# Kernel tuning notes

Hardware: AMD Instinct MI355X
Metric: run time of the kernel (lower is better)

Reference implementation:

```python
import jax, jax.numpy as jnp
import numpy as np

N, C, P, K = 100000, 64, 64, 16  # points, in_planes, planes, nsample
EPS = 1e-5

def _bn(y, g, b, m, v):
    # inference-mode batchnorm over channel (last) dim
    return (y - m) * (g * jax.lax.rsqrt(v + EPS)) + b

def setup_inputs() -> dict:
    key = jax.random.key(0)
    ks = jax.random.split(key, 12)
    p = jax.random.normal(ks[0], (N, 3), jnp.float32)
    x = jax.random.normal(ks[1], (N, C), jnp.float32)
    idx = jax.random.randint(ks[2], (N, K), 0, N, jnp.int32)
    s = 0.05
    w1 = jax.random.normal(ks[3], (C, P), jnp.float32) * s
    conv_w = jax.random.normal(ks[4], (P, P + 3), jnp.float32) * s  # Conv1d(P+3, P, 1) weight squeezed
    w3 = jax.random.normal(ks[5], (P, P), jnp.float32) * s
    def bn_params(k):
        k1, k2 = jax.random.split(k)
        return (jnp.ones((P,), jnp.float32),                      # gamma
                jnp.zeros((P,), jnp.float32),                     # beta
                jax.random.normal(k1, (P,), jnp.float32) * 0.01,  # running mean
                jnp.abs(jax.random.normal(k2, (P,), jnp.float32)) * 0.1 + 1.0)  # running var
    g1, b1, m1, v1 = bn_params(ks[6])
    g2, b2, m2, v2 = bn_params(ks[7])
    g3, b3, m3, v3 = bn_params(ks[8])
    return dict(p=p, x=x, idx=idx, w1=w1, g1=g1, b1=b1, m1=m1, v1=v1,
                conv_w=conv_w, g2=g2, b2=b2, m2=m2, v2=v2,
                w3=w3, g3=g3, b3=b3, m3=m3, v3=v3)

def reference(p, x, idx, w1, g1, b1, m1, v1, conv_w, g2, b2, m2, v2, w3, g3, b3, m3, v3):
    identity = x
    h = jax.nn.relu(_bn(x @ w1, g1, b1, m1, v1))                     # [N, P]
    # queryandgroup with use_xyz=True: concat(relative xyz, neighbor feats)
    rel = p[idx] - p[:, None, :]                                      # [N, K, 3]
    grouped = jnp.concatenate([rel, h[idx]], axis=-1)                 # [N, K, 3+P]
    e = jnp.einsum('nkc,oc->nko', grouped, conv_w)                    # conv1x1 -> [N, K, P]
    e = jax.nn.relu(_bn(e, g2, b2, m2, v2))
    f = jnp.max(e, axis=1)                                            # max over neighbors -> [N, P]
    out = jax.nn.relu(_bn(f @ w3, g3, b3, m3, v3) + identity)         # [N, P]
    return out
```

## Files before the change

kernel.cpp:

```cpp
#include <hip/hip_runtime.h>
#include <stdint.h>


#define EPS 1e-5f

typedef unsigned short u16;
typedef unsigned int u32;
typedef __attribute__((ext_vector_type(8))) short bf16x8;
typedef __attribute__((ext_vector_type(4))) float f32x4;

__device__ __forceinline__ float b2f(u16 u) { return __uint_as_float(((u32)u) << 16); }
__device__ __forceinline__ u16 f2b(float f) {
    u32 u = __float_as_uint(f);
    u32 r = u + 0x7fffu + ((u >> 16) & 1u);
    return (u16)(r >> 16);
}
__device__ __forceinline__ bool is_bf16(const void* g) { return ((const u32*)g)[0] == 0x3F803F80u; }
__device__ __forceinline__ float ldval(const void* p, size_t i, bool isbf) {
    return isbf ? b2f(((const u16*)p)[i]) : ((const float*)p)[i];
}
#define MFMA16(a, b, c) __builtin_amdgcn_mfma_f32_16x16x32_bf16(a, b, c, 0, 0, 0)

__device__ __forceinline__ bf16x8 asbf(uint4 u) {
    union { uint4 u; bf16x8 b; } c;
    c.u = u;
    return c.b;
}

__device__ __forceinline__ bf16x8 ldrow8(const void* base, size_t row, int coff, bool isbf) {
    if (isbf) {
        const u16* pp = (const u16*)base + row * 64 + coff;
        return asbf(*(const uint4*)pp);
    } else {
        const float* pp = (const float*)base + row * 64 + coff;
        float4 q0 = ((const float4*)pp)[0], q1 = ((const float4*)pp)[1];
        bf16x8 r;
        r[0] = (short)f2b(q0.x); r[1] = (short)f2b(q0.y);
        r[2] = (short)f2b(q0.z); r[3] = (short)f2b(q0.w);
        r[4] = (short)f2b(q1.x); r[5] = (short)f2b(q1.y);
        r[6] = (short)f2b(q1.z); r[7] = (short)f2b(q1.w);
        return r;
    }
}

__global__ void __launch_bounds__(256)
k_prep(const void* __restrict__ w1, const void* __restrict__ cw, const void* __restrict__ w3,
       const void* __restrict__ g1, const void* __restrict__ b1, const void* __restrict__ m1,
       const void* __restrict__ v1, const void* __restrict__ g2, const void* __restrict__ b2,
       const void* __restrict__ m2, const void* __restrict__ v2, const void* __restrict__ g3,
       const void* __restrict__ b3, const void* __restrict__ m3, const void* __restrict__ v3,
       uint4* __restrict__ w1f, uint4* __restrict__ cwf, uint4* __restrict__ w3f,
       float* __restrict__ bnst) {
    const bool isbf = is_bf16(g1);
    const int tid = blockIdx.x * blockDim.x + threadIdx.x;
    if (tid < 512) {
        int f = tid >> 6, lane = tid & 63;
        int ch = f >> 2, t = f & 3, quad = lane >> 4, c0 = lane & 15;
        union { uint4 u; bf16x8 b; } r;
#pragma unroll
        for (int j = 0; j < 8; ++j) {
            int c = ch * 32 + quad * 8 + j, o = t * 16 + c0;
            r.b[j] = (short)f2b(ldval(w1, (size_t)c * 64 + o, isbf));
        }
        w1f[f * 64 + lane] = r.u;
    } else if (tid < 1280) {
        int f = (tid - 512) >> 6, lane = tid & 63;
        int ch = f >> 2, t = f & 3, quad = lane >> 4, c0 = lane & 15;
        union { uint4 u; bf16x8 b; } r;
#pragma unroll
        for (int j = 0; j < 8; ++j) {
            int o = t * 16 + c0;
            short val;
            if (ch < 2) {
                int c = ch * 32 + quad * 8 + j;
                val = (short)f2b(ldval(cw, (size_t)o * 67 + 3 + c, isbf));
            } else {
                int pc = quad * 8 + j;
                val = (pc < 3) ? (short)f2b(ldval(cw, (size_t)o * 67 + pc, isbf)) : (short)0;
            }
            r.b[j] = val;
        }
        cwf[f * 64 + lane] = r.u;
    } else if (tid < 1792) {
        int f = (tid - 1280) >> 6, lane = tid & 63;
        int ch = f >> 2, t = f & 3, quad = lane >> 4, c0 = lane & 15;
        union { uint4 u; bf16x8 b; } r;
#pragma unroll
        for (int j = 0; j < 8; ++j) {
            int c = ch * 32 + quad * 8 + j, o = t * 16 + c0;
            r.b[j] = (short)f2b(ldval(w3, (size_t)c * 64 + o, isbf));
        }
        w3f[f * 64 + lane] = r.u;
    } else if (tid < 2176) {
        int id = tid - 1792;
        int bn = id >> 7, rem = id & 127, ch = rem & 63, which = rem >> 6;
        const void* g = (bn == 0) ? g1 : (bn == 1) ? g2 : g3;
        const void* b = (bn == 0) ? b1 : (bn == 1) ? b2 : b3;
        const void* m = (bn == 0) ? m1 : (bn == 1) ? m2 : m3;
        const void* v = (bn == 0) ? v1 : (bn == 1) ? v2 : v3;
        float gv = ldval(g, ch, isbf), bv = ldval(b, ch, isbf);
        float mv = ldval(m, ch, isbf), vv = ldval(v, ch, isbf);
        float s = gv * rsqrtf(vv + EPS);
        float t = bv - mv * s;
        bnst[bn * 128 + which * 64 + ch] = which ? t : s;
    }
}

__global__ void __launch_bounds__(256, 4)
k_h_mfma(const void* __restrict__ x, const void* __restrict__ p, const void* __restrict__ g1,
         const uint4* __restrict__ w1f, const float* __restrict__ bnst,
         float4* __restrict__ p4, u16* __restrict__ hbf, int N) {
    const bool isbf = is_bf16(g1);
    const int lane = threadIdx.x & 63, quad = lane >> 4, col = lane & 15;
    const int wave = blockIdx.x * (blockDim.x >> 6) + (threadIdx.x >> 6);
    const int nw = gridDim.x * (blockDim.x >> 6);
    bf16x8 B00 = asbf(w1f[0 * 64 + lane]), B01 = asbf(w1f[1 * 64 + lane]);
    bf16x8 B02 = asbf(w1f[2 * 64 + lane]), B03 = asbf(w1f[3 * 64 + lane]);
    bf16x8 B10 = asbf(w1f[4 * 64 + lane]), B11 = asbf(w1f[5 * 64 + lane]);
    bf16x8 B12 = asbf(w1f[6 * 64 + lane]), B13 = asbf(w1f[7 * 64 + lane]);
    f32x4 sv, tv;
#pragma unroll
    for (int t = 0; t < 4; ++t) {
        sv[t] = bnst[0 * 128 + 0 + t * 16 + col];
        tv[t] = bnst[0 * 128 + 64 + t * 16 + col];
    }
    const int nt = (N + 15) >> 4;
    for (int ti = wave; ti < nt; ti += nw) {
        const int n0 = ti * 16;
        int ra = n0 + col;
        if (ra > N - 1) ra = N - 1;
        bf16x8 A0 = ldrow8(x, (size_t)ra, quad * 8, isbf);
        bf16x8 A1 = ldrow8(x, (size_t)ra, 32 + quad * 8, isbf);
        if (p4 && quad == 0 && n0 + col < N) {
            int row = n0 + col;
            float4 pv;
            pv.x = ldval(p, (size_t)row * 3 + 0, isbf);
            pv.y = ldval(p, (size_t)row * 3 + 1, isbf);
            pv.z = ldval(p, (size_t)row * 3 + 2, isbf);
            pv.w = 0.f;
            p4[row] = pv;
        }
        f32x4 acc0 = {0.f, 0.f, 0.f, 0.f}, acc1 = acc0, acc2 = acc0, acc3 = acc0;
        acc0 = MFMA16(A0, B00, acc0); acc0 = MFMA16(A1, B10, acc0);
        acc1 = MFMA16(A0, B01, acc1); acc1 = MFMA16(A1, B11, acc1);
        acc2 = MFMA16(A0, B02, acc2); acc2 = MFMA16(A1, B12, acc2);
        acc3 = MFMA16(A0, B03, acc3); acc3 = MFMA16(A1, B13, acc3);
#define STT(acc, t)                                                            \
    {                                                                          \
        _Pragma("unroll") for (int r = 0; r < 4; ++r) {                        \
            int row = n0 + quad * 4 + r;                                       \
            if (row < N) {                                                     \
                float e = acc[r] * sv[t] + tv[t];                              \
                hbf[(size_t)row * 64 + (t)*16 + col] = f2b(fmaxf(e, 0.f));     \
            }                                                                  \
        }                                                                      \
    }
        STT(acc0, 0) STT(acc1, 1) STT(acc2, 2) STT(acc3, 3)
#undef STT
    }
}

__global__ void __launch_bounds__(256, 4)
k_w_mfma(u16* __restrict__ hw, u16* __restrict__ vbuf, const void* __restrict__ p,
         const void* __restrict__ g1, const uint4* __restrict__ cwf, int N) {
    const bool isbf = is_bf16(g1);
    const int lane = threadIdx.x & 63, quad = lane >> 4, col = lane & 15;
    const int wave = blockIdx.x * (blockDim.x >> 6) + (threadIdx.x >> 6);
    const int nw = gridDim.x * (blockDim.x >> 6);
    bf16x8 B00 = asbf(cwf[0 * 64 + lane]), B01 = asbf(cwf[1 * 64 + lane]);
    bf16x8 B02 = asbf(cwf[2 * 64 + lane]), B03 = asbf(cwf[3 * 64 + lane]);
    bf16x8 B10 = asbf(cwf[4 * 64 + lane]), B11 = asbf(cwf[5 * 64 + lane]);
    bf16x8 B12 = asbf(cwf[6 * 64 + lane]), B13 = asbf(cwf[7 * 64 + lane]);
    bf16x8 B20 = asbf(cwf[8 * 64 + lane]), B21 = asbf(cwf[9 * 64 + lane]);
    bf16x8 B22 = asbf(cwf[10 * 64 + lane]), B23 = asbf(cwf[11 * 64 + lane]);
    const int nt = (N + 15) >> 4;
    for (int ti = wave; ti < nt; ti += nw) {
        const int n0 = ti * 16;
        int ra = n0 + col;
        if (ra > N - 1) ra = N - 1;
        bf16x8 A0 = asbf(*(const uint4*)(hw + (size_t)ra * 64 + quad * 8));
        bf16x8 A1 = asbf(*(const uint4*)(hw + (size_t)ra * 64 + 32 + quad * 8));
        bf16x8 A2 = {0, 0, 0, 0, 0, 0, 0, 0};
        if (quad == 0) {
            A2[0] = (short)f2b(ldval(p, (size_t)ra * 3 + 0, isbf));
            A2[1] = (short)f2b(ldval(p, (size_t)ra * 3 + 1, isbf));
            A2[2] = (short)f2b(ldval(p, (size_t)ra * 3 + 2, isbf));
        }
        f32x4 z = {0.f, 0.f, 0.f, 0.f};
        f32x4 av0 = MFMA16(A2, B20, z), av1 = MFMA16(A2, B21, z);
        f32x4 av2 = MFMA16(A2, B22, z), av3 = MFMA16(A2, B23, z);
        f32x4 aw0 = MFMA16(A1, B10, MFMA16(A0, B00, av0));
        f32x4 aw1 = MFMA16(A1, B11, MFMA16(A0, B01, av1));
        f32x4 aw2 = MFMA16(A1, B12, MFMA16(A0, B02, av2));
        f32x4 aw3 = MFMA16(A1, B13, MFMA16(A0, B03, av3));
#define STW(accv, accw, t)                                                     \
    {                                                                          \
        _Pragma("unroll") for (int r = 0; r < 4; ++r) {                        \
            int row = n0 + quad * 4 + r;                                       \
            if (row < N) {                                                     \
                vbuf[(size_t)row * 64 + (t)*16 + col] = f2b(accv[r]);          \
                hw[(size_t)row * 64 + (t)*16 + col] = f2b(accw[r]);            \
            }                                                                  \
        }                                                                      \
    }
        STW(av0, aw0, 0) STW(av1, aw1, 1) STW(av2, aw2, 2) STW(av3, aw3, 3)
#undef STW
    }
}

__global__ void __launch_bounds__(256, 5)
k_gmax(const u16* __restrict__ wbuf, u16* __restrict__ vf, const int* __restrict__ idx,
       const float* __restrict__ bnst, int N) {
    const int lane = threadIdx.x & 63;
    const int wave = blockIdx.x * (blockDim.x >> 6) + (threadIdx.x >> 6);
    const int nw = gridDim.x * (blockDim.x >> 6);
    const float s2 = bnst[128 + lane];
    const float t2 = bnst[192 + lane];
    const int step = 4 * nw;
    int i = 4 * wave;
    if (i >= N) return;
    const size_t idxmax = (size_t)N * 16 - 1;
    size_t a0 = (size_t)i * 16 + lane;
    int jv = idx[a0 > idxmax ? idxmax : a0];
    for (; i < N; i += step) {
        size_t an = (size_t)(i + step) * 16 + lane;
        int jn = idx[an > idxmax ? idxmax : an];
        u32 wr0[16], wr1[16], wr2[16], wr3[16];
#pragma unroll
        for (int k = 0; k < 16; ++k) {
            int j0 = __builtin_amdgcn_readlane(jv, k);
            int j1 = __builtin_amdgcn_readlane(jv, 16 + k);
            int j2 = __builtin_amdgcn_readlane(jv, 32 + k);
            int j3 = __builtin_amdgcn_readlane(jv, 48 + k);
            wr0[k] = wbuf[(size_t)j0 * 64 + lane];
            wr1[k] = wbuf[(size_t)j1 * 64 + lane];
            wr2[k] = wbuf[(size_t)j2 * 64 + lane];
            wr3[k] = wbuf[(size_t)j3 * 64 + lane];
        }
        const int i1 = (i + 1 < N) ? i + 1 : i;
        const int i2 = (i + 2 < N) ? i + 2 : i;
        const int i3 = (i + 3 < N) ? i + 3 : i;
        u32 v0 = vf[(size_t)i * 64 + lane];
        u32 v1 = vf[(size_t)i1 * 64 + lane];
        u32 v2 = vf[(size_t)i2 * 64 + lane];
        u32 v3 = vf[(size_t)i3 * 64 + lane];
#define REDST(wr, vv, row, guard)                                              \
    {                                                                          \
        float mx = b2f((u16)wr[0]), mn = mx;                                   \
        _Pragma("unroll") for (int k = 1; k < 16; ++k) {                       \
            float fv_ = b2f((u16)wr[k]);                                       \
            mx = fmaxf(mx, fv_);                                               \
            mn = fminf(mn, fv_);                                               \
        }                                                                      \
        float e = fmaxf(s2 * mx, s2 * mn) + t2 - s2 * b2f((u16)vv);            \
        if (guard) vf[(size_t)(row)*64 + lane] = f2b(fmaxf(e, 0.f));           \
    }
        REDST(wr0, v0, i, true)
        REDST(wr1, v1, i + 1, (i + 1 < N))
        REDST(wr2, v2, i + 2, (i + 2 < N))
        REDST(wr3, v3, i + 3, (i + 3 < N))
#undef REDST
        jv = jn;
    }
}

template <bool FORCE_BF16>
__global__ void __launch_bounds__(256, 4)
k_conv_mfma(const u16* __restrict__ hbf, const float4* __restrict__ p4,
            const int* __restrict__ idx, const uint4* __restrict__ cwf,
            const float* __restrict__ bnst, const void* __restrict__ g2,
            void* __restrict__ fout, int N) {
    const bool isbf = is_bf16(g2);
    const int lane = threadIdx.x & 63, quad = lane >> 4, col = lane & 15;
    const int wave = blockIdx.x * (blockDim.x >> 6) + (threadIdx.x >> 6);
    const int nw = gridDim.x * (blockDim.x >> 6);
    bf16x8 B00 = asbf(cwf[0 * 64 + lane]), B01 = asbf(cwf[1 * 64 + lane]);
    bf16x8 B02 = asbf(cwf[2 * 64 + lane]), B03 = asbf(cwf[3 * 64 + lane]);
    bf16x8 B10 = asbf(cwf[4 * 64 + lane]), B11 = asbf(cwf[5 * 64 + lane]);
    bf16x8 B12 = asbf(cwf[6 * 64 + lane]), B13 = asbf(cwf[7 * 64 + lane]);
    bf16x8 B20 = asbf(cwf[8 * 64 + lane]), B21 = asbf(cwf[9 * 64 + lane]);
    bf16x8 B22 = asbf(cwf[10 * 64 + lane]), B23 = asbf(cwf[11 * 64 + lane]);
    f32x4 sv, tv;
#pragma unroll
    for (int t = 0; t < 4; ++t) {
        sv[t] = bnst[1 * 128 + 0 + t * 16 + col];
        tv[t] = bnst[1 * 128 + 64 + t * 16 + col];
    }
    int i = wave;
    if (i >= N) return;
    const int step = nw;
    int i1 = i + step;
    int i1c = (i1 < N) ? i1 : N - 1;
    int j0 = idx[(size_t)i * 16 + col];
    int j1 = idx[(size_t)i1c * 16 + col];
    const uint4* r0 = (const uint4*)(hbf + (size_t)j0 * 64);
    uint4 h0_c = r0[quad], h1_c = r0[4 + quad];
    float4 pj_c = p4[j0];
    float4 pn_c = p4[i];
    for (; i < N; i += step, i1 += step) {
        const int i2 = i1 + step;
        const int i2c = (i2 < N) ? i2 : N - 1;
        int j2 = idx[(size_t)i2c * 16 + col];
        const uint4* rn = (const uint4*)(hbf + (size_t)j1 * 64);
        uint4 h0_n = rn[quad], h1_n = rn[4 + quad];
        const int i1cc = (i1 < N) ? i1 : N - 1;
        float4 pj_n = p4[j1];
        float4 pn_n = p4[i1cc];
        bf16x8 A2 = {0, 0, 0, 0, 0, 0, 0, 0};
        if (quad == 0) {
            A2[0] = (short)f2b(pj_c.x - pn_c.x);
            A2[1] = (short)f2b(pj_c.y - pn_c.y);
            A2[2] = (short)f2b(pj_c.z - pn_c.z);
        }
        f32x4 z = {0.f, 0.f, 0.f, 0.f};
        f32x4 acc0 = z, acc1 = z, acc2 = z, acc3 = z;
        bf16x8 a0 = asbf(h0_c), a1 = asbf(h1_c);
        acc0 = MFMA16(a0, B00, acc0);
        acc1 = MFMA16(a0, B01, acc1);
        acc2 = MFMA16(a0, B02, acc2);
        acc3 = MFMA16(a0, B03, acc3);
        acc0 = MFMA16(a1, B10, acc0);
        acc1 = MFMA16(a1, B11, acc1);
        acc2 = MFMA16(a1, B12, acc2);
        acc3 = MFMA16(a1, B13, acc3);
        acc0 = MFMA16(A2, B20, acc0);
        acc1 = MFMA16(A2, B21, acc1);
        acc2 = MFMA16(A2, B22, acc2);
        acc3 = MFMA16(A2, B23, acc3);
#define RED(acc, t, dst)                                                       \
    {                                                                          \
        float mx = fmaxf(fmaxf(acc[0], acc[1]), fmaxf(acc[2], acc[3]));        \
        float mn = fminf(fminf(acc[0], acc[1]), fminf(acc[2], acc[3]));        \
        mx = fmaxf(mx, __shfl_xor(mx, 16));                                    \
        mn = fminf(mn, __shfl_xor(mn, 16));                                    \
        mx = fmaxf(mx, __shfl_xor(mx, 32));                                    \
        mn = fminf(mn, __shfl_xor(mn, 32));                                    \
        float e = fmaxf(sv[t] * mx + tv[t], sv[t] * mn + tv[t]);               \
        dst = fmaxf(e, 0.f);                                                   \
    }
        float f0, f1, f2, f3;
        RED(acc0, 0, f0) RED(acc1, 1, f1) RED(acc2, 2, f2) RED(acc3, 3, f3)
#undef RED
        float fv = (lane < 16) ? f0 : (lane < 32) ? f1 : (lane < 48) ? f2 : f3;
        if (FORCE_BF16 || isbf)
            ((u16*)fout)[(size_t)i * 64 + lane] = f2b(fv);
        else
            ((float*)fout)[(size_t)i * 64 + lane] = fv;
        j0 = j1; j1 = j2;
        h0_c = h0_n; h1_c = h1_n;
        pj_c = pj_n; pn_c = pn_n;
    }
}

template <bool FIN_BF16_ALWAYS>
__global__ void __launch_bounds__(256, 4)
k_out_mfma(const void* __restrict__ fin, const void* __restrict__ x,
           const uint4* __restrict__ w3f, const float* __restrict__ bnst,
           const void* __restrict__ g3, void* __restrict__ out, int N) {
    const bool isbf = is_bf16(g3);
    const bool finbf = FIN_BF16_ALWAYS ? true : isbf;
    const int lane = threadIdx.x & 63, quad = lane >> 4, col = lane & 15;
    const int wave = blockIdx.x * (blockDim.x >> 6) + (threadIdx.x >> 6);
    const int nw = gridDim.x * (blockDim.x >> 6);
    bf16x8 B00 = asbf(w3f[0 * 64 + lane]), B01 = asbf(w3f[1 * 64 + lane]);
    bf16x8 B02 = asbf(w3f[2 * 64 + lane]), B03 = asbf(w3f[3 * 64 + lane]);
    bf16x8 B10 = asbf(w3f[4 * 64 + lane]), B11 = asbf(w3f[5 * 64 + lane]);
    bf16x8 B12 = asbf(w3f[6 * 64 + lane]), B13 = asbf(w3f[7 * 64 + lane]);
    f32x4 sv, tv;
#pragma unroll
    for (int t = 0; t < 4; ++t) {
        sv[t] = bnst[2 * 128 + 0 + t * 16 + col];
        tv[t] = bnst[2 * 128 + 64 + t * 16 + col];
    }
    const int nt = (N + 15) >> 4;
    for (int ti = wave; ti < nt; ti += nw) {
        const int n0 = ti * 16;
        int ra = n0 + col;
        if (ra > N - 1) ra = N - 1;
        bf16x8 A0 = ldrow8(fin, (size_t)ra, quad * 8, finbf);
        bf16x8 A1 = ldrow8(fin, (size_t)ra, 32 + quad * 8, finbf);
        f32x4 acc0 = {0.f, 0.f, 0.f, 0.f}, acc1 = acc0, acc2 = acc0, acc3 = acc0;
        acc0 = MFMA16(A0, B00, acc0); acc0 = MFMA16(A1, B10, acc0);
        acc1 = MFMA16(A0, B01, acc1); acc1 = MFMA16(A1, B11, acc1);
        acc2 = MFMA16(A0, B02, acc2); acc2 = MFMA16(A1, B12, acc2);
        acc3 = MFMA16(A0, B03, acc3); acc3 = MFMA16(A1, B13, acc3);
#define STT(acc, t)                                                            \
    {                                                                          \
        _Pragma("unroll") for (int r = 0; r < 4; ++r) {                        \
            int row = n0 + quad * 4 + r;                                       \
            if (row < N) {                                                     \
                int o_ = (t)*16 + col;                                         \
                float e = acc[r] * sv[t] + tv[t] +                             \
                          ldval(x, (size_t)row * 64 + o_, isbf);               \
                e = fmaxf(e, 0.f);                                             \
                if (isbf)                                                      \
                    ((u16*)out)[(size_t)row * 64 + o_] = f2b(e);               \
                else                                                           \
                    ((float*)out)[(size_t)row * 64 + o_] = e;                  \
            }                                                                  \
        }                                                                      \
    }
        STT(acc0, 0) STT(acc1, 1) STT(acc2, 2) STT(acc3, 3)
#undef STT
    }
}

__device__ __forceinline__ void load_col64(const void* w, int lane, bool isbf, float* col) {
#pragma unroll
    for (int c = 0; c < 64; ++c) col[c] = ldval(w, (size_t)c * 64 + lane, isbf);
}
__device__ __forceinline__ float dot64(const void* x, size_t off, bool isbf, const float* col) {
    float a0 = 0.f;
#pragma unroll
    for (int c = 0; c < 64; ++c) a0 += ldval(x, off + c, isbf) * col[c];
    return a0;
}
__device__ __forceinline__ void bn_st(const void* g, const void* b, const void* m,
                                      const void* v, int o, bool isbf, float& s, float& t) {
    float gv = ldval(g, o, isbf), bv = ldval(b, o, isbf);
    float mv = ldval(m, o, isbf), vv = ldval(v, o, isbf);
    s = gv * rsqrtf(vv + EPS);
    t = bv - mv * s;
}
__global__ void __launch_bounds__(256) k_mono(const void* __restrict__ p, const void* __restrict__ x,
                                              const int* __restrict__ idx, const void* __restrict__ w1,
                                              const void* __restrict__ g1, const void* __restrict__ b1,
                                              const void* __restrict__ m1, const void* __restrict__ v1,
                                              const void* __restrict__ cw, const void* __restrict__ g2,
                                              const void* __restrict__ b2, const void* __restrict__ m2,
                                              const void* __restrict__ v2, const void* __restrict__ w3,
                                              const void* __restrict__ g3, const void* __restrict__ b3,
                                              const void* __restrict__ m3, const void* __restrict__ v3,
                                              void* __restrict__ out, int N) {
    const bool isbf = is_bf16(g1);
    const int lane = threadIdx.x & 63;
    const int wave = blockIdx.x * (blockDim.x >> 6) + (threadIdx.x >> 6);
    const int nw = gridDim.x * (blockDim.x >> 6);
    float w1col[64];
    load_col64(w1, lane, isbf, w1col);
    float w3col[64];
    load_col64(w3, lane, isbf, w3col);
    float s1, t1, s2, t2, s3, t3;
    bn_st(g1, b1, m1, v1, lane, isbf, s1, t1);
    bn_st(g2, b2, m2, v2, lane, isbf, s2, t2);
    bn_st(g3, b3, m3, v3, lane, isbf, s3, t3);
    for (int n = wave; n < N; n += nw) {
        const int4* ir = (const int4*)(idx + (size_t)n * 16);
        float pnx = ldval(p, (size_t)n * 3 + 0, isbf);
        float pny = ldval(p, (size_t)n * 3 + 1, isbf);
        float pnz = ldval(p, (size_t)n * 3 + 2, isbf);
        float fmx = 0.f;
        for (int kk = 0; kk < 4; ++kk) {
            const int4 iv = ir[kk];
#pragma unroll
            for (int t = 0; t < 4; ++t) {
                const int j = (t == 0) ? iv.x : (t == 1) ? iv.y : (t == 2) ? iv.z : iv.w;
                float hr = dot64(x, (size_t)j * 64, isbf, w1col);
                float hv = fmaxf(hr * s1 + t1, 0.f);
                float a0 = (ldval(p, (size_t)j * 3 + 0, isbf) - pnx) * ldval(cw, (size_t)lane * 67 + 0, isbf) +
                           (ldval(p, (size_t)j * 3 + 1, isbf) - pny) * ldval(cw, (size_t)lane * 67 + 1, isbf) +
                           (ldval(p, (size_t)j * 3 + 2, isbf) - pnz) * ldval(cw, (size_t)lane * 67 + 2, isbf);
#pragma unroll
                for (int c = 0; c < 64; ++c)
                    a0 += __shfl(hv, c) * ldval(cw, (size_t)lane * 67 + 3 + c, isbf);
                fmx = fmaxf(fmx, a0 * s2 + t2);
            }
        }
        float a = 0.f;
#pragma unroll
        for (int c = 0; c < 64; ++c) a += __shfl(fmx, c) * w3col[c];
        float r = a * s3 + t3 + ldval(x, (size_t)n * 64 + lane, isbf);
        r = fmaxf(r, 0.f);
        if (isbf)
            ((u16*)out)[(size_t)n * 64 + lane] = f2b(r);
        else
            ((float*)out)[(size_t)n * 64 + lane] = r;
    }
}

extern "C" void kernel_launch(void* const* d_in, const int* in_sizes, int n_in,
                              void* d_out, int out_size, void* d_ws, size_t ws_size,
                              hipStream_t stream) {
    const void* p = d_in[0];
    const void* x = d_in[1];
    const int* idx = (const int*)d_in[2];
    const void* w1 = d_in[3];
    const void* g1 = d_in[4];
    const void* b1 = d_in[5];
    const void* m1 = d_in[6];
    const void* v1 = d_in[7];
    const void* cw = d_in[8];
    const void* g2 = d_in[9];
    const void* b2 = d_in[10];
    const void* m2 = d_in[11];
    const void* v2 = d_in[12];
    const void* w3 = d_in[13];
    const void* g3 = d_in[14];
    const void* b3 = d_in[15];
    const void* m3 = d_in[16];
    const void* v3 = d_in[17];
    const int N = in_sizes[0] / 3;

    const int blk = 256;
    const int nt = (N + 15) >> 4;
    const int gh = (nt + 3) >> 2;
    const int gg = 1280;

    const size_t hb = (size_t)N * 64 * sizeof(u16);
    const size_t p4b = (size_t)N * sizeof(float4);
    const size_t packb = 8192 + 12288 + 8192 + 1536;
    const size_t need_big = 256 + 2 * hb + packb;
    const size_t need_h = 256 + hb + p4b + packb;

    if (ws_size >= need_big) {
        char* base = (char*)d_ws + 256;
        u16* b1buf = (u16*)base;
        u16* b2buf = (u16*)(base + hb);
        char* rest = base + 2 * hb;
        uint4* w1f = (uint4*)rest;
        uint4* cwf = (uint4*)(rest + 8192);
        uint4* w3f = (uint4*)(rest + 8192 + 12288);
        float* bnst = (float*)(rest + 8192 + 12288 + 8192);
        k_prep<<<9, blk, 0, stream>>>(w1, cw, w3, g1, b1, m1, v1, g2, b2, m2, v2,
                                      g3, b3, m3, v3, w1f, cwf, w3f, bnst);
        k_h_mfma<<<gh, blk, 0, stream>>>(x, p, g1, w1f, bnst, nullptr, b1buf, N);
        k_w_mfma<<<gh, blk, 0, stream>>>(b1buf, b2buf, p, g1, cwf, N);
        k_gmax<<<gg, blk, 0, stream>>>(b1buf, b2buf, idx, bnst, N);
        k_out_mfma<true><<<gh, blk, 0, stream>>>((const void*)b2buf, x, w3f, bnst, g3,
                                                 d_out, N);
    } else if (ws_size >= need_h) {
        char* base = (char*)d_ws + 256;
        u16* h = (u16*)base;
        char* rest = base + hb;
        float4* p4 = (float4*)rest;
        uint4* w1f = (uint4*)(rest + p4b);
        uint4* cwf = (uint4*)(rest + p4b + 8192);
        uint4* w3f = (uint4*)(rest + p4b + 8192 + 12288);
        float* bnst = (float*)(rest + p4b + 8192 + 12288 + 8192);
        k_prep<<<9, blk, 0, stream>>>(w1, cw, w3, g1, b1, m1, v1, g2, b2, m2, v2,
                                      g3, b3, m3, v3, w1f, cwf, w3f, bnst);
        k_h_mfma<<<gh, blk, 0, stream>>>(x, p, g1, w1f, bnst, p4, h, N);
        k_conv_mfma<false><<<2048, blk, 0, stream>>>(h, p4, idx, cwf, bnst, g2, d_out, N);
        k_out_mfma<false><<<gh, blk, 0, stream>>>((const void*)d_out, x, w3f, bnst, g3,
                                                  d_out, N);
    } else {
        k_mono<<<2048, blk, 0, stream>>>(p, x, idx, w1, g1, b1, m1, v1, cw, g2, b2, m2, v2,
                                         w3, g3, b3, m3, v3, d_out, N);
    }
}
```

Measured before the change: 173.9 us.

## Fuse first linear layer and conv-weight projection into one kernel via LDS

Merges the x@w1+BN+ReLU kernel with the per-point conv projection kernel, passing the h tile between MFMA stages through a per-wave shared-memory buffer instead of global memory. This removes one kernel launch and a full N×64 bf16 write and re-read of h. The fused kernel holds more weight fragments in registers, so launch bounds drop to 3 blocks per CU, which may reduce occupancy.

```diff
diff --git a/kernel.cpp b/kernel.cpp
--- a/kernel.cpp
+++ b/kernel.cpp
@@ -103,6 +103,84 @@
         float s = gv * rsqrtf(vv + EPS);
         float t = bv - mv * s;
         bnst[bn * 128 + which * 64 + ch] = which ? t : s;
+    }
+}
+
+__global__ void __launch_bounds__(256, 3)
+k_hw_mfma(const void* __restrict__ x, const void* __restrict__ p, const void* __restrict__ g1,
+          const uint4* __restrict__ w1f, const uint4* __restrict__ cwf,
+          const float* __restrict__ bnst, u16* __restrict__ wbuf, u16* __restrict__ vbuf,
+          int N) {
+    const bool isbf = is_bf16(g1);
+    const int lane = threadIdx.x & 63, quad = lane >> 4, col = lane & 15;
+    const int wv = threadIdx.x >> 6;
+    const int wave = blockIdx.x * (blockDim.x >> 6) + wv;
+    const int nw = gridDim.x * (blockDim.x >> 6);
+    __shared__ u16 hlds[4][16][72];
+    f32x4 sv, tv;
+#pragma unroll
+    for (int t = 0; t < 4; ++t) {
+        sv[t] = bnst[0 * 128 + 0 + t * 16 + col];
+        tv[t] = bnst[0 * 128 + 64 + t * 16 + col];
+    }
+    bf16x8 W00 = asbf(w1f[0 * 64 + lane]), W01 = asbf(w1f[1 * 64 + lane]);
+    bf16x8 W02 = asbf(w1f[2 * 64 + lane]), W03 = asbf(w1f[3 * 64 + lane]);
+    bf16x8 W10 = asbf(w1f[4 * 64 + lane]), W11 = asbf(w1f[5 * 64 + lane]);
+    bf16x8 W12 = asbf(w1f[6 * 64 + lane]), W13 = asbf(w1f[7 * 64 + lane]);
+    bf16x8 B00 = asbf(cwf[0 * 64 + lane]), B01 = asbf(cwf[1 * 64 + lane]);
+    bf16x8 B02 = asbf(cwf[2 * 64 + lane]), B03 = asbf(cwf[3 * 64 + lane]);
+    bf16x8 B10 = asbf(cwf[4 * 64 + lane]), B11 = asbf(cwf[5 * 64 + lane]);
+    bf16x8 B12 = asbf(cwf[6 * 64 + lane]), B13 = asbf(cwf[7 * 64 + lane]);
+    bf16x8 B20 = asbf(cwf[8 * 64 + lane]), B21 = asbf(cwf[9 * 64 + lane]);
+    bf16x8 B22 = asbf(cwf[10 * 64 + lane]), B23 = asbf(cwf[11 * 64 + lane]);
+    const int nt = (N + 15) >> 4;
+    for (int ti = wave; ti < nt; ti += nw) {
+        const int n0 = ti * 16;
+        int ra = n0 + col;
+        if (ra > N - 1) ra = N - 1;
+        bf16x8 A0 = ldrow8(x, (size_t)ra, quad * 8, isbf);
+        bf16x8 A1 = ldrow8(x, (size_t)ra, 32 + quad * 8, isbf);
+        f32x4 hc0 = {0.f, 0.f, 0.f, 0.f}, hc1 = hc0, hc2 = hc0, hc3 = hc0;
+        hc0 = MFMA16(A0, W00, hc0); hc0 = MFMA16(A1, W10, hc0);
+        hc1 = MFMA16(A0, W01, hc1); hc1 = MFMA16(A1, W11, hc1);
+        hc2 = MFMA16(A0, W02, hc2); hc2 = MFMA16(A1, W12, hc2);
+        hc3 = MFMA16(A0, W03, hc3); hc3 = MFMA16(A1, W13, hc3);
+#define HST(acc, t)                                                            \
+    {                                                                          \
+        _Pragma("unroll") for (int r = 0; r < 4; ++r) {                        \
+            hlds[wv][quad * 4 + r][(t)*16 + col] =                             \
+                f2b(fmaxf(acc[r] * sv[t] + tv[t], 0.f));                       \
+        }                                                                      \
+    }
+        HST(hc0, 0) HST(hc1, 1) HST(hc2, 2) HST(hc3, 3)
+#undef HST
+        bf16x8 hA0 = asbf(*(const uint4*)&hlds[wv][lane & 15][(lane >> 4) * 8]);
+        bf16x8 hA1 = asbf(*(const uint4*)&hlds[wv][lane & 15][32 + (lane >> 4) * 8]);
+        bf16x8 A2 = {0, 0, 0, 0, 0, 0, 0, 0};
+        if (quad == 0) {
+            A2[0] = (short)f2b(ldval(p, (size_t)ra * 3 + 0, isbf));
+            A2[1] = (short)f2b(ldval(p, (size_t)ra * 3 + 1, isbf));
+            A2[2] = (short)f2b(ldval(p, (size_t)ra * 3 + 2, isbf));
+        }
+        f32x4 z = {0.f, 0.f, 0.f, 0.f};
+        f32x4 av0 = MFMA16(A2, B20, z), av1 = MFMA16(A2, B21, z);
+        f32x4 av2 = MFMA16(A2, B22, z), av3 = MFMA16(A2, B23, z);
+        f32x4 aw0 = MFMA16(hA1, B10, MFMA16(hA0, B00, av0));
+        f32x4 aw1 = MFMA16(hA1, B11, MFMA16(hA0, B01, av1));
+        f32x4 aw2 = MFMA16(hA1, B12, MFMA16(hA0, B02, av2));
+        f32x4 aw3 = MFMA16(hA1, B13, MFMA16(hA0, B03, av3));
+#define STW(accv, accw, t)                                                     \
+    {                                                                          \
+        _Pragma("unroll") for (int r = 0; r < 4; ++r) {                        \
+            int row = n0 + quad * 4 + r;                                       \
+            if (row < N) {                                                     \
+                vbuf[(size_t)row * 64 + (t)*16 + col] = f2b(accv[r]);          \
+                wbuf[(size_t)row * 64 + (t)*16 + col] = f2b(accw[r]);          \
+            }                                                                  \
+        }                                                                      \
+    }
+        STW(av0, aw0, 0) STW(av1, aw1, 1) STW(av2, aw2, 2) STW(av3, aw3, 3)
+#undef STW
     }
 }
 
@@ -157,54 +235,6 @@
     }
         STT(acc0, 0) STT(acc1, 1) STT(acc2, 2) STT(acc3, 3)
 #undef STT
-    }
-}
-
-__global__ void __launch_bounds__(256, 4)
-k_w_mfma(u16* __restrict__ hw, u16* __restrict__ vbuf, const void* __restrict__ p,
-         const void* __restrict__ g1, const uint4* __restrict__ cwf, int N) {
-    const bool isbf = is_bf16(g1);
-    const int lane = threadIdx.x & 63, quad = lane >> 4, col = lane & 15;
-    const int wave = blockIdx.x * (blockDim.x >> 6) + (threadIdx.x >> 6);
-    const int nw = gridDim.x * (blockDim.x >> 6);
-    bf16x8 B00 = asbf(cwf[0 * 64 + lane]), B01 = asbf(cwf[1 * 64 + lane]);
-    bf16x8 B02 = asbf(cwf[2 * 64 + lane]), B03 = asbf(cwf[3 * 64 + lane]);
-    bf16x8 B10 = asbf(cwf[4 * 64 + lane]), B11 = asbf(cwf[5 * 64 + lane]);
-    bf16x8 B12 = asbf(cwf[6 * 64 + lane]), B13 = asbf(cwf[7 * 64 + lane]);
-    bf16x8 B20 = asbf(cwf[8 * 64 + lane]), B21 = asbf(cwf[9 * 64 + lane]);
-    bf16x8 B22 = asbf(cwf[10 * 64 + lane]), B23 = asbf(cwf[11 * 64 + lane]);
-    const int nt = (N + 15) >> 4;
-    for (int ti = wave; ti < nt; ti += nw) {
-        const int n0 = ti * 16;
-        int ra = n0 + col;
-        if (ra > N - 1) ra = N - 1;
-        bf16x8 A0 = asbf(*(const uint4*)(hw + (size_t)ra * 64 + quad * 8));
-        bf16x8 A1 = asbf(*(const uint4*)(hw + (size_t)ra * 64 + 32 + quad * 8));
-        bf16x8 A2 = {0, 0, 0, 0, 0, 0, 0, 0};
-        if (quad == 0) {
-            A2[0] = (short)f2b(ldval(p, (size_t)ra * 3 + 0, isbf));
-            A2[1] = (short)f2b(ldval(p, (size_t)ra * 3 + 1, isbf));
-            A2[2] = (short)f2b(ldval(p, (size_t)ra * 3 + 2, isbf));
-        }
-        f32x4 z = {0.f, 0.f, 0.f, 0.f};
-        f32x4 av0 = MFMA16(A2, B20, z), av1 = MFMA16(A2, B21, z);
-        f32x4 av2 = MFMA16(A2, B22, z), av3 = MFMA16(A2, B23, z);
-        f32x4 aw0 = MFMA16(A1, B10, MFMA16(A0, B00, av0));
-        f32x4 aw1 = MFMA16(A1, B11, MFMA16(A0, B01, av1));
-        f32x4 aw2 = MFMA16(A1, B12, MFMA16(A0, B02, av2));
-        f32x4 aw3 = MFMA16(A1, B13, MFMA16(A0, B03, av3));
-#define STW(accv, accw, t)                                                     \
-    {                                                                          \
-        _Pragma("unroll") for (int r = 0; r < 4; ++r) {                        \
-            int row = n0 + quad * 4 + r;                                       \
-            if (row < N) {                                                     \
-                vbuf[(size_t)row * 64 + (t)*16 + col] = f2b(accv[r]);          \
-                hw[(size_t)row * 64 + (t)*16 + col] = f2b(accw[r]);            \
-            }                                                                  \
-        }                                                                      \
-    }
-        STW(av0, aw0, 0) STW(av1, aw1, 1) STW(av2, aw2, 2) STW(av3, aw3, 3)
-#undef STW
     }
 }
 
@@ -523,8 +553,7 @@
         float* bnst = (float*)(rest + 8192 + 12288 + 8192);
         k_prep<<<9, blk, 0, stream>>>(w1, cw, w3, g1, b1, m1, v1, g2, b2, m2, v2,
                                       g3, b3, m3, v3, w1f, cwf, w3f, bnst);
-        k_h_mfma<<<gh, blk, 0, stream>>>(x, p, g1, w1f, bnst, nullptr, b1buf, N);
-        k_w_mfma<<<gh, blk, 0, stream>>>(b1buf, b2buf, p, g1, cwf, N);
+        k_hw_mfma<<<gh, blk, 0, stream>>>(x, p, g1, w1f, cwf, bnst, b1buf, b2buf, N);
         k_gmax<<<gg, blk, 0, stream>>>(b1buf, b2buf, idx, bnst, N);
         k_out_mfma<true><<<gh, blk, 0, stream>>>((const void*)b2buf, x, w3f, bnst, g3,
                                                  d_out, N);
```

Result: faster. 170.2 us (-2.2%).
